# Kernel tuning notes

Measured on AMD Instinct MI355X. Metric: run time of the kernel, lower is better.

Reference implementation:

```python
import jax, jax.numpy as jnp
import numpy as np

D = 3  # hardcoded window half-width in the module


def setup_inputs() -> dict:
    key = jax.random.key(0)
    ks = jax.random.split(key, 5)
    B, T, S = 16, 1024, 4096
    q_size, c_size, p_size = 512, 512, 512
    q = jax.random.normal(ks[0], (B, q_size, S), jnp.float32)
    c_t = jax.random.normal(ks[1], (B, T, c_size), jnp.float32)
    # torch nn.Linear weight layouts: (out_features, in_features)
    W_a = jax.random.normal(ks[2], (c_size, q_size), jnp.float32) / np.sqrt(q_size).astype(np.float32)
    W_p = jax.random.normal(ks[3], (p_size, c_size), jnp.float32) / np.sqrt(c_size).astype(np.float32)
    V_p = jax.random.normal(ks[4], (1, p_size), jnp.float32) / np.sqrt(p_size).astype(np.float32)
    return {"q": q, "c_t": c_t, "W_a": W_a, "W_p": W_p, "V_p": V_p}


def reference(q, c_t, W_a, W_p, V_p):
    B, q_size, S = q.shape
    # predictive alignment: p_t = S * sigmoid(V_p tanh(W_p c_t)) -> (B, T, 1)
    p_t = S * jax.nn.sigmoid(jnp.tanh(c_t @ W_p.T) @ V_p.T)
    # pad one NaN column at the front of the sequence, then (B, S+1, q_size)
    q_pad = jnp.pad(q, ((0, 0), (0, 0), (1, 0)), constant_values=jnp.nan).transpose(0, 2, 1)
    # window indices: clamp(long(p_t) + idx + 1, 0, S+1) % (S+1), idx in [-D, D]
    offsets = jnp.arange(-D + 1, D + 2)  # (2D+1,)
    s = jnp.clip(p_t.astype(jnp.int32) + offsets[None, None, :], 0, S + 1) % (S + 1)  # (B,T,2D+1)
    # per-batch gather of the local window: (B, T, 2D+1, q_size)
    qg = q_pad[jnp.arange(B)[:, None, None], s]
    nan_loc = jnp.isnan(qg[..., 0])  # (B, T, 2D+1)
    qg = jnp.where(nan_loc[..., None], 0.0, qg)
    # score: dot(W_a q, c_t) -> (B, T, 2D+1)
    a_t = jnp.einsum('btwq,cq,btc->btw', qg, W_a, c_t)
    a_t = jnp.where(nan_loc, -jnp.inf, a_t)
    attn = jax.nn.softmax(a_t, axis=2)
    # Gaussian decay around predicted position p_t
    gauss = jnp.exp(-2.0 * ((jnp.clip(s.astype(jnp.float32) - 1.0, 0.0, None) - p_t) / D) ** 2)
    W_attn = attn * gauss
    out = jnp.einsum('btw,btwq->btq', W_attn, qg)  # (B, T, q_size)
    return out
```

## Files before the change

### kernel.cpp

```cpp
#include <hip/hip_runtime.h>
#include <hip/hip_bf16.h>

#define BB 16
#define TT 1024
#define SS 4096
#define CS 512
#define QS 512
#define PS 512
#define NROW (BB*TT)

typedef unsigned short ushort_t;
typedef unsigned int u32;
typedef short bf16x8 __attribute__((ext_vector_type(8)));
typedef float f32x4 __attribute__((ext_vector_type(4)));

#define AS1 __attribute__((address_space(1)))
#define AS3 __attribute__((address_space(3)))

__device__ __forceinline__ void gl2l16(const void* g, void* l) {
    __builtin_amdgcn_global_load_lds((const AS1 u32*)g, (AS3 u32*)l, 16, 0, 0);
}

__device__ __forceinline__ ushort_t f2bf(float f) {
    u32 x = __float_as_uint(f);
    return (ushort_t)((x + 0x7fffu + ((x >> 16) & 1u)) >> 16);
}
__device__ __forceinline__ float bf2f(ushort_t b) {
    return __uint_as_float(((u32)b) << 16);
}

__global__ __launch_bounds__(256) void k_conv_a(const float* __restrict__ c,
                                                ushort_t* __restrict__ A) {
    const int i = blockIdx.x * 256 + threadIdx.x;
    const int m = i >> 7;
    const int k = (i & 127) * 4;
    float4 v = *(const float4*)(c + (size_t)m * CS + k);
    ushort4 hi, lo;
    hi.x = f2bf(v.x); lo.x = f2bf(v.x - bf2f(hi.x));
    hi.y = f2bf(v.y); lo.y = f2bf(v.y - bf2f(hi.y));
    hi.z = f2bf(v.z); lo.z = f2bf(v.z - bf2f(hi.z));
    hi.w = f2bf(v.w); lo.w = f2bf(v.w - bf2f(hi.w));
    *(ushort4*)(A + (size_t)m * 1024 + k)       = hi;
    *(ushort4*)(A + (size_t)m * 1024 + 512 + k) = lo;
}

__global__ __launch_bounds__(256) void k_conv_b(const float* __restrict__ Wa,
                                                const float* __restrict__ Wp,
                                                ushort_t* __restrict__ B,
                                                int* __restrict__ cnt) {
    const int n = blockIdx.x;
    const int t = threadIdx.x;
    if (n == 0 && t < 2) cnt[t] = 0;
    #pragma unroll
    for (int kk = 0; kk < 2; ++kk) {
        const int k = t + 256 * kk;
        float v = (n < 512) ? Wa[(size_t)k * QS + n] : Wp[(size_t)(n - 512) * CS + k];
        ushort_t hi = f2bf(v);
        ushort_t lo = f2bf(v - bf2f(hi));
        B[(size_t)n * 1024 + k]       = hi;
        B[(size_t)n * 1024 + 512 + k] = lo;
    }
}

__global__ __launch_bounds__(256) void k_tq(const float* __restrict__ q,
                                            float* __restrict__ qT) {
    const int b  = blockIdx.z;
    const int s0 = blockIdx.x * 64 + (threadIdx.x & 15) * 4;
    const int d0 = blockIdx.y * 64 + (threadIdx.x >> 4) * 4;
    const float* qb = q + ((size_t)b * QS + d0) * SS + s0;
    float4 v0 = *(const float4*)(qb);
    float4 v1 = *(const float4*)(qb + SS);
    float4 v2 = *(const float4*)(qb + 2 * SS);
    float4 v3 = *(const float4*)(qb + 3 * SS);
    float* qo = qT + ((size_t)b * SS + s0) * QS + d0;
    *(float4*)(qo)          = make_float4(v0.x, v1.x, v2.x, v3.x);
    *(float4*)(qo + QS)     = make_float4(v0.y, v1.y, v2.y, v3.y);
    *(float4*)(qo + 2 * QS) = make_float4(v0.z, v1.z, v2.z, v3.z);
    *(float4*)(qo + 3 * QS) = make_float4(v0.w, v1.w, v2.w, v3.w);
}

__global__ __launch_bounds__(1024, 4) void k_gemm(const ushort_t* __restrict__ A,
                                                  const ushort_t* __restrict__ B,
                                                  const float* __restrict__ V_p,
                                                  float* __restrict__ u,
                                                  float* __restrict__ zpart) {
    __shared__ ushort_t lds[8][8192];
    const int tid = threadIdx.x;
    const int l = tid & 63;
    const int w = tid >> 6;
    const int wm = w >> 2;
    const int wn = w & 3;
    const int ln = l & 15, lh = l >> 4;

    const int orig = blockIdx.x;
    const int swz = ((orig & 7) << 5) + (orig >> 3);
    const int m0 = (swz >> 2) * 256;
    const int nt = swz & 3;
    const int n0 = nt * 256;

    const int srow = tid >> 2;
    const int scg  = tid & 3;
    const int scol0 = (scg ^ ((srow >> 1) & 3)) * 8;

    const int swzr = (lh ^ ((ln >> 1) & 3)) << 3;
    int aoffL[4], boffL[4];
    #pragma unroll
    for (int mi = 0; mi < 4; ++mi)
        aoffL[mi] = (wm * 64 + mi * 16 + ln) * 32 + swzr;
    #pragma unroll
    for (int ni = 0; ni < 4; ++ni)
        boffL[ni] = (wn * 64 + ni * 16 + ln) * 32 + swzr;

    f32x4 acc[4][4];
    #pragma unroll
    for (int a = 0; a < 4; ++a)
        #pragma unroll
        for (int b2 = 0; b2 < 4; ++b2) acc[a][b2] = (f32x4){0.f, 0.f, 0.f, 0.f};

    auto STAGE = [&](int c) {
        const int tt = c >> 2, rem = c & 3, kh = rem >> 1;
        const int blk = tt >> 3, k0 = (tt & 7) << 6;
        const ushort_t* src;
        if (rem & 1) {
            const int boff = (blk == 1) ? 512 : 0;
            src = B + (size_t)(n0 + srow) * 1024 + boff + k0 + kh * 32 + scol0;
        } else {
            const int aoff = (blk == 2) ? 512 : 0;
            src = A + (size_t)(m0 + srow) * 1024 + aoff + k0 + kh * 32 + scol0;
        }
        gl2l16(src, &lds[c & 7][tid * 8]);
    };

    #pragma unroll
    for (int c = 0; c < 6; ++c) STAGE(c);
    asm volatile("s_waitcnt vmcnt(2)" ::: "memory");
    __builtin_amdgcn_s_barrier();

    #pragma unroll 1
    for (int t = 0; t < 24; ++t) {
        #pragma unroll
        for (int P = 0; P < 2; ++P) {
            const int sA = ((t << 2) + (P << 1)) & 7;
            const int sB = sA + 1;
            const ushort_t* bA = &lds[sA][0];
            const ushort_t* bB = &lds[sB][0];
            bf16x8 af[4], bb[4];
            #pragma unroll
            for (int mi = 0; mi < 4; ++mi)
                af[mi] = *(const bf16x8*)(bA + aoffL[mi]);
            #pragma unroll
            for (int ni = 0; ni < 4; ++ni)
                bb[ni] = *(const bf16x8*)(bB + boffL[ni]);
            const int c0 = (t << 2) + (P << 1) + 6;
            if (c0 <= 95) STAGE(c0);
            if (c0 + 1 <= 95) STAGE(c0 + 1);
            __builtin_amdgcn_s_setprio(1);
            #pragma unroll
            for (int mi = 0; mi < 4; ++mi)
                #pragma unroll
                for (int ni = 0; ni < 4; ++ni)
                    acc[mi][ni] = __builtin_amdgcn_mfma_f32_16x16x32_bf16(
                        af[mi], bb[ni], acc[mi][ni], 0, 0, 0);
            __builtin_amdgcn_s_setprio(0);
            if (P == 1) {
                if (t == 22) { asm volatile("s_waitcnt vmcnt(0)" ::: "memory"); }
                else if (t < 22) { asm volatile("s_waitcnt vmcnt(2)" ::: "memory"); }
            }
            __builtin_amdgcn_s_barrier();
        }
    }

    if (nt < 2) {
        #pragma unroll
        for (int mi = 0; mi < 4; ++mi) {
            #pragma unroll
            for (int r = 0; r < 4; ++r) {
                const int m = m0 + wm * 64 + mi * 16 + lh * 4 + r;
                float* up = u + (size_t)m * QS + nt * 256 + wn * 64 + ln;
                #pragma unroll
                for (int ni = 0; ni < 4; ++ni) up[ni * 16] = acc[mi][ni][r];
            }
        }
    } else {
        float vp[4];
        #pragma unroll
        for (int ni = 0; ni < 4; ++ni)
            vp[ni] = V_p[(nt - 2) * 256 + wn * 64 + ni * 16 + ln];
        #pragma unroll
        for (int mi = 0; mi < 4; ++mi) {
            #pragma unroll
            for (int r = 0; r < 4; ++r) {
                float sv = 0.f;
                #pragma unroll
                for (int ni = 0; ni < 4; ++ni) sv += tanhf(acc[mi][ni][r]) * vp[ni];
                sv += __shfl_xor(sv, 1, 64);
                sv += __shfl_xor(sv, 2, 64);
                sv += __shfl_xor(sv, 4, 64);
                sv += __shfl_xor(sv, 8, 64);
                if (ln == 0)
                    zpart[(size_t)(m0 + wm * 64 + mi * 16 + lh * 4 + r) * 8 +
                          (nt - 2) * 4 + wn] = sv;
            }
        }
    }
}

__global__ __launch_bounds__(256) void k_z(const float* __restrict__ zpart,
                                           float* __restrict__ pt, int* __restrict__ tr,
                                           int* __restrict__ list1, int* __restrict__ cnt1) {
    const int row = blockIdx.x * 256 + threadIdx.x;
    const float4 a = *(const float4*)(zpart + (size_t)row * 8);
    const float4 b = *(const float4*)(zpart + (size_t)row * 8 + 4);
    float z = ((a.x + a.y) + (a.z + a.w)) + ((b.x + b.y) + (b.z + b.w));
    float ptv = 4096.f / (1.f + expf(-z));
    float fr = ptv - floorf(ptv);
    pt[row] = ptv;
    tr[row] = (int)ptv;
    if (fr < 0.06f || fr > 0.94f) {
        int i = atomicAdd(cnt1, 1);
        list1[i] = row;
    }
}

__global__ __launch_bounds__(256) void k_rep1(
    const float* __restrict__ c_t, const float* __restrict__ W_p,
    const float* __restrict__ V_p, float* __restrict__ pt, int* __restrict__ tr,
    const int* __restrict__ list1, const int* __restrict__ cnt1,
    int* __restrict__ list2, int* __restrict__ cnt2)
{
    const int tid = threadIdx.x;
    const int lane = tid & 63;
    const int wid = tid >> 6;
    const int n1 = cnt1[0];
    __shared__ float cl[8][132 * 4];
    __shared__ double zl[4][8];
    __shared__ int rows_s[8];

    for (int g0 = blockIdx.x * 8; g0 < n1; g0 += gridDim.x * 8) {
        const int nr = min(8, n1 - g0);
        __syncthreads();
        if (tid < nr) rows_s[tid] = list1[g0 + tid];
        __syncthreads();
        for (int idx = tid; idx < nr * 128; idx += 256) {
            int r = idx >> 7, k = (idx & 127) * 4;
            *(float4*)&cl[r][k] = *(const float4*)(c_t + (size_t)rows_s[r] * CS + k);
        }
        __syncthreads();

        const float* wp0 = W_p + (size_t)tid * CS;
        const float* wp1 = W_p + (size_t)(tid + 256) * CS;
        f32x4 acc[2][8];
        #pragma unroll
        for (int p = 0; p < 2; ++p)
            #pragma unroll
            for (int r = 0; r < 8; ++r) acc[p][r] = (f32x4){0.f, 0.f, 0.f, 0.f};

        for (int k = 0; k < CS; k += 16) {
            f32x4 w0[4], w1[4];
            #pragma unroll
            for (int j = 0; j < 4; ++j) {
                w0[j] = *(const f32x4*)(wp0 + k + 4 * j);
                w1[j] = *(const f32x4*)(wp1 + k + 4 * j);
            }
            #pragma unroll
            for (int j = 0; j < 4; ++j) {
                #pragma unroll
                for (int r = 0; r < 8; ++r) {
                    f32x4 c4 = *(const f32x4*)&cl[r][k + 4 * j];
                    acc[0][r] += c4 * w0[j];
                    acc[1][r] += c4 * w1[j];
                }
            }
        }

        const float vp0 = V_p[tid];
        const float vp1 = V_p[tid + 256];
        double zp[8];
        #pragma unroll
        for (int r = 0; r < 8; ++r) {
            float X0 = (acc[0][r][0] + acc[0][r][1]) + (acc[0][r][2] + acc[0][r][3]);
            float X1 = (acc[1][r][0] + acc[1][r][1]) + (acc[1][r][2] + acc[1][r][3]);
            zp[r] = (double)(tanhf(X0) * vp0) + (double)(tanhf(X1) * vp1);
        }
        #pragma unroll
        for (int r = 0; r < 8; ++r) {
            double v = zp[r];
            #pragma unroll
            for (int o = 32; o > 0; o >>= 1) v += __shfl_down(v, o, 64);
            if (lane == 0) zl[wid][r] = v;
        }
        __syncthreads();
        if (tid < nr) {
            double z = (zl[0][tid] + zl[1][tid]) + (zl[2][tid] + zl[3][tid]);
            double ptv = 4096.0 / (1.0 + exp(-z));
            const int row = rows_s[tid];
            pt[row] = (float)ptv;
            tr[row] = (int)ptv;
            double fr = ptv - floor(ptv);
            if (fr < 5e-3 || fr > 0.995) {
                int i2 = atomicAdd(cnt2, 1);
                list2[i2] = row;
            }
        }
    }
}

__global__ __launch_bounds__(256) void k_rep2a(
    const float* __restrict__ c_t, const float* __restrict__ W_p,
    const float* __restrict__ V_p,
    const int* __restrict__ list2, const int* __restrict__ cnt2,
    double* __restrict__ zp2)
{
    const int tid = threadIdx.x;
    const int pl = tid & 63;
    const int kq = tid >> 6;
    const int n2 = cnt2[0];
    __shared__ float cl[CS];
    __shared__ double xsh[4][64];

    for (int i = blockIdx.x; i < n2 * 8; i += gridDim.x) {
        const int li = i >> 3;
        const int pc = i & 7;
        const int row = list2[li];
        const int p0 = pc * 64;
        __syncthreads();
        if (tid < 128)
            *(float4*)(cl + tid * 4) = *(const float4*)(c_t + (size_t)row * CS + tid * 4);
        __syncthreads();
        const float* wr = W_p + (size_t)(p0 + pl) * CS + kq * 128;
        const float* cr = cl + kq * 128;
        double Xa = 0.0, Xb = 0.0, Xc = 0.0, Xd = 0.0;
        #pragma unroll 4
        for (int k = 0; k < 128; k += 4) {
            float4 w4 = *(const float4*)(wr + k);
            float4 c4 = *(const float4*)(cr + k);
            Xa += (double)c4.x * w4.x;
            Xb += (double)c4.y * w4.y;
            Xc += (double)c4.z * w4.z;
            Xd += (double)c4.w * w4.w;
        }
        xsh[kq][pl] = (Xa + Xb) + (Xc + Xd);
        __syncthreads();
        if (tid < 64) {
            double X = (xsh[0][pl] + xsh[1][pl]) + (xsh[2][pl] + xsh[3][pl]);
            double zv = tanh(X) * (double)V_p[p0 + pl];
            #pragma unroll
            for (int o = 32; o > 0; o >>= 1) zv += __shfl_down(zv, o, 64);
            if (pl == 0) zp2[i] = zv;
        }
    }
}

__global__ __launch_bounds__(256) void k_rep2b(
    const double* __restrict__ zp2, const int* __restrict__ list2,
    const int* __restrict__ cnt2, float* __restrict__ pt, int* __restrict__ tr)
{
    const int idx = blockIdx.x * 256 + threadIdx.x;
    if (idx >= cnt2[0]) return;
    const double* zr = zp2 + (size_t)idx * 8;
    double z = 0.0;
    #pragma unroll
    for (int j = 0; j < 8; ++j) z += zr[j];
    double ptv = 4096.0 / (1.0 + exp(-z));
    const int row = list2[idx];
    pt[row] = (float)ptv;
    tr[row] = (int)ptv;
}

__global__ __launch_bounds__(256) void k_attn_t(
    const float* __restrict__ qT, const float* __restrict__ u,
    const float* __restrict__ pt, const int* __restrict__ tr,
    float* __restrict__ out)
{
    const int wid = threadIdx.x >> 6;
    const int lane = threadIdx.x & 63;
    const int bt = blockIdx.x * 4 + wid;
    const int b = bt >> 10;

    const float* urow = u + (size_t)bt * QS;
    float4 ua = *(const float4*)(urow + lane * 8);
    float4 ub = *(const float4*)(urow + lane * 8 + 4);
    float uv[8] = {ua.x, ua.y, ua.z, ua.w, ub.x, ub.y, ub.z, ub.w};

    const float ptv = pt[bt];
    const int tn = tr[bt];
    const float* qTb = qT + (size_t)b * SS * QS;

    bool val[7];
    int pos[7];
    #pragma unroll
    for (int w = 0; w < 7; ++w) {
        int sv = tn + w - 2;
        sv = sv < 0 ? 0 : (sv > SS + 1 ? SS + 1 : sv);
        if (sv == SS + 1) sv = 0;
        val[w] = (sv != 0);
        pos[w] = sv - 1;
    }

    float qg[7][8];
    #pragma unroll
    for (int w = 0; w < 7; ++w) {
        if (val[w]) {
            const float* qr = qTb + (size_t)pos[w] * QS + lane * 8;
            float4 a = *(const float4*)qr;
            float4 c = *(const float4*)(qr + 4);
            qg[w][0] = a.x; qg[w][1] = a.y; qg[w][2] = a.z; qg[w][3] = a.w;
            qg[w][4] = c.x; qg[w][5] = c.y; qg[w][6] = c.z; qg[w][7] = c.w;
        } else {
            #pragma unroll
            for (int j = 0; j < 8; ++j) qg[w][j] = 0.f;
        }
    }

    float at[7];
    #pragma unroll
    for (int w = 0; w < 7; ++w) {
        float p = 0.f;
        #pragma unroll
        for (int j = 0; j < 8; ++j) p = fmaf(qg[w][j], uv[j], p);
        #pragma unroll
        for (int o = 1; o < 64; o <<= 1) p += __shfl_xor(p, o, 64);
        at[w] = p;
    }

    float m = -1e30f;
    #pragma unroll
    for (int w = 0; w < 7; ++w) if (val[w]) m = fmaxf(m, at[w]);
    float e[7], den = 0.f;
    #pragma unroll
    for (int w = 0; w < 7; ++w) { e[w] = val[w] ? expf(at[w] - m) : 0.f; den += e[w]; }
    const float inv = 1.f / den;

    float acc[8] = {0.f, 0.f, 0.f, 0.f, 0.f, 0.f, 0.f, 0.f};
    #pragma unroll
    for (int w = 0; w < 7; ++w) {
        if (val[w]) {
            float d = ((float)pos[w] - ptv) * (1.f / 3.f);
            float wt = e[w] * inv * expf(-2.f * d * d);
            #pragma unroll
            for (int j = 0; j < 8; ++j) acc[j] = fmaf(wt, qg[w][j], acc[j]);
        }
    }

    float* orow = out + (size_t)bt * QS + lane * 8;
    *(float4*)orow       = make_float4(acc[0], acc[1], acc[2], acc[3]);
    *(float4*)(orow + 4) = make_float4(acc[4], acc[5], acc[6], acc[7]);
}

__global__ __launch_bounds__(256) void k_attn_g(
    const float* __restrict__ q, const float* __restrict__ u,
    const float* __restrict__ pt, const int* __restrict__ tr,
    float* __restrict__ out)
{
    const int wid = threadIdx.x >> 6;
    const int lane = threadIdx.x & 63;
    const int bt = blockIdx.x * 4 + wid;
    const int b = bt >> 10;

    const float* urow = u + (size_t)bt * QS;
    float4 ua = *(const float4*)(urow + lane * 8);
    float4 ub = *(const float4*)(urow + lane * 8 + 4);
    float uv[8] = {ua.x, ua.y, ua.z, ua.w, ub.x, ub.y, ub.z, ub.w};

    const float ptv = pt[bt];
    const int tn = tr[bt];
    const float* qb = q + (size_t)b * QS * SS;

    bool val[7];
    int pos[7];
    #pragma unroll
    for (int w = 0; w < 7; ++w) {
        int sv = tn + w - 2;
        sv = sv < 0 ? 0 : (sv > SS + 1 ? SS + 1 : sv);
        if (sv == SS + 1) sv = 0;
        val[w] = (sv != 0);
        pos[w] = sv - 1;
    }

    float qg[7][8];
    #pragma unroll
    for (int j = 0; j < 8; ++j) {
        const float* qrow = qb + (size_t)(lane * 8 + j) * SS;
        #pragma unroll
        for (int w = 0; w < 7; ++w)
            qg[w][j] = val[w] ? qrow[pos[w]] : 0.f;
    }

    float at[7];
    #pragma unroll
    for (int w = 0; w < 7; ++w) {
        float p = 0.f;
        #pragma unroll
        for (int j = 0; j < 8; ++j) p = fmaf(qg[w][j], uv[j], p);
        #pragma unroll
        for (int o = 1; o < 64; o <<= 1) p += __shfl_xor(p, o, 64);
        at[w] = p;
    }

    float m = -1e30f;
    #pragma unroll
    for (int w = 0; w < 7; ++w) if (val[w]) m = fmaxf(m, at[w]);
    float e[7], den = 0.f;
    #pragma unroll
    for (int w = 0; w < 7; ++w) { e[w] = val[w] ? expf(at[w] - m) : 0.f; den += e[w]; }
    const float inv = 1.f / den;

    float acc[8] = {0.f, 0.f, 0.f, 0.f, 0.f, 0.f, 0.f, 0.f};
    #pragma unroll
    for (int w = 0; w < 7; ++w) {
        if (val[w]) {
            float d = ((float)pos[w] - ptv) * (1.f / 3.f);
            float wt = e[w] * inv * expf(-2.f * d * d);
            #pragma unroll
            for (int j = 0; j < 8; ++j) acc[j] = fmaf(wt, qg[w][j], acc[j]);
        }
    }

    float* orow = out + (size_t)bt * QS + lane * 8;
    *(float4*)orow       = make_float4(acc[0], acc[1], acc[2], acc[3]);
    *(float4*)(orow + 4) = make_float4(acc[4], acc[5], acc[6], acc[7]);
}

extern "C" void kernel_launch(void* const* d_in, const int* in_sizes, int n_in,
                              void* d_out, int out_size, void* d_ws, size_t ws_size,
                              hipStream_t stream) {
    const float* q   = (const float*)d_in[0];
    const float* c_t = (const float*)d_in[1];
    const float* W_a = (const float*)d_in[2];
    const float* W_p = (const float*)d_in[3];
    const float* V_p = (const float*)d_in[4];
    float* out = (float*)d_out;

    char* ws = (char*)d_ws;
    ushort_t* Ap  = (ushort_t*)(ws);
    ushort_t* Bp  = (ushort_t*)(ws + 33554432);
    float*    u   = (float*)  (ws + 35651584);
    float*    zp  = (float*)  (ws + 69206016);
    float*    pt  = (float*)  (ws + 69730304);
    int*      tr  = (int*)    (ws + 69795840);
    int*      l1  = (int*)    (ws + 69861376);
    int*      l2  = (int*)    (ws + 69926912);
    int*      cnt = (int*)    (ws + 69992448);
    double*   zp2 = (double*) (ws + 70000640);
    float*    qT  = (float*)  (ws + 73400320);
    const bool use_T = (ws_size >= 73400320ULL + 134217728ULL);

    hipLaunchKernelGGL(k_conv_a, dim3(8192), dim3(256), 0, stream, c_t, Ap);
    hipLaunchKernelGGL(k_conv_b, dim3(1024), dim3(256), 0, stream, W_a, W_p, Bp, cnt);
    hipLaunchKernelGGL(k_gemm, dim3(256), dim3(1024), 0, stream, Ap, Bp, V_p, u, zp);
    hipLaunchKernelGGL(k_z, dim3(64), dim3(256), 0, stream, zp, pt, tr, l1, cnt);
    hipLaunchKernelGGL(k_rep1, dim3(512), dim3(256), 0, stream,
                       c_t, W_p, V_p, pt, tr, l1, cnt, l2, cnt + 1);
    hipLaunchKernelGGL(k_rep2a, dim3(512), dim3(256), 0, stream,
                       c_t, W_p, V_p, l2, cnt + 1, zp2);
    hipLaunchKernelGGL(k_rep2b, dim3(64), dim3(256), 0, stream,
                       zp2, l2, cnt + 1, pt, tr);
    if (use_T) {
        hipLaunchKernelGGL(k_tq, dim3(64, 8, 16), dim3(256), 0, stream, q, qT);
        hipLaunchKernelGGL(k_attn_t, dim3(NROW / 4), dim3(256), 0, stream, qT, u, pt, tr, out);
    } else {
        hipLaunchKernelGGL(k_attn_g, dim3(NROW / 4), dim3(256), 0, stream, q, u, pt, tr, out);
    }
}
```

Before: 240.9 us.

## Restructure GEMM LDS pipeline to one barrier per four-chunk iteration

Changes the global-to-LDS staging schedule in the projection GEMM. The old code prefetched six chunks ahead and had two half-steps per iteration, each ending with a barrier. The new code stages a full group of four chunks for the next iteration up front, computes both halves, then does a full vmcnt(0) wait and a single barrier per iteration. This halves the barrier count, but the prefetch distance drops to one iteration and the full wait may expose load latency.

```diff
diff --git a/kernel.cpp b/kernel.cpp
--- a/kernel.cpp
+++ b/kernel.cpp
@@ -132,18 +132,19 @@
     };
 
     #pragma unroll
-    for (int c = 0; c < 6; ++c) STAGE(c);
-    asm volatile("s_waitcnt vmcnt(2)" ::: "memory");
+    for (int c = 0; c < 4; ++c) STAGE(c);
+    asm volatile("s_waitcnt vmcnt(0)" ::: "memory");
     __builtin_amdgcn_s_barrier();
 
     #pragma unroll 1
     for (int t = 0; t < 24; ++t) {
-        #pragma unroll
-        for (int P = 0; P < 2; ++P) {
-            const int sA = ((t << 2) + (P << 1)) & 7;
-            const int sB = sA + 1;
-            const ushort_t* bA = &lds[sA][0];
-            const ushort_t* bB = &lds[sB][0];
+        if (t < 23) {
+            #pragma unroll
+            for (int i = 0; i < 4; ++i) STAGE(4 * t + 4 + i);
+        }
+        {
+            const ushort_t* bA = &lds[(4 * t) & 7][0];
+            const ushort_t* bB = &lds[(4 * t + 1) & 7][0];
             bf16x8 af[4], bb[4];
             #pragma unroll
             for (int mi = 0; mi < 4; ++mi)
@@ -151,9 +152,6 @@
             #pragma unroll
             for (int ni = 0; ni < 4; ++ni)
                 bb[ni] = *(const bf16x8*)(bB + boffL[ni]);
-            const int c0 = (t << 2) + (P << 1) + 6;
-            if (c0 <= 95) STAGE(c0);
-            if (c0 + 1 <= 95) STAGE(c0 + 1);
             __builtin_amdgcn_s_setprio(1);
             #pragma unroll
             for (int mi = 0; mi < 4; ++mi)
@@ -162,12 +160,28 @@
                     acc[mi][ni] = __builtin_amdgcn_mfma_f32_16x16x32_bf16(
                         af[mi], bb[ni], acc[mi][ni], 0, 0, 0);
             __builtin_amdgcn_s_setprio(0);
-            if (P == 1) {
-                if (t == 22) { asm volatile("s_waitcnt vmcnt(0)" ::: "memory"); }
-                else if (t < 22) { asm volatile("s_waitcnt vmcnt(2)" ::: "memory"); }
-            }
-            __builtin_amdgcn_s_barrier();
-        }
+        }
+        {
+            const ushort_t* bA = &lds[(4 * t + 2) & 7][0];
+            const ushort_t* bB = &lds[(4 * t + 3) & 7][0];
+            bf16x8 af[4], bb[4];
+            #pragma unroll
+            for (int mi = 0; mi < 4; ++mi)
+                af[mi] = *(const bf16x8*)(bA + aoffL[mi]);
+            #pragma unroll
+            for (int ni = 0; ni < 4; ++ni)
+                bb[ni] = *(const bf16x8*)(bB + boffL[ni]);
+            __builtin_amdgcn_s_setprio(1);
+            #pragma unroll
+            for (int mi = 0; mi < 4; ++mi)
+                #pragma unroll
+                for (int ni = 0; ni < 4; ++ni)
+                    acc[mi][ni] = __builtin_amdgcn_mfma_f32_16x16x32_bf16(
+                        af[mi], bb[ni], acc[mi][ni], 0, 0, 0);
+            __builtin_amdgcn_s_setprio(0);
+        }
+        asm volatile("s_waitcnt vmcnt(0)" ::: "memory");
+        __builtin_amdgcn_s_barrier();
     }
 
     if (nt < 2) {
```

After: 238.8 us. About the same (-0.9%).
